# Kernel optimization log

Hardware: AMD Instinct MI355X
Metric: run time of the kernel (lower is better)

The kernel has to match this reference:

```python
import jax, jax.numpy as jnp
import numpy as np

N_NODES = 100000
NODES_PER_GRAPH = 200
N_GRAPHS = N_NODES // NODES_PER_GRAPH  # 500
N_EDGES = 3200000
NUM_FEATURES = 128
HIDDEN = 32
K_POOL = 50
NUM_CLASSES = 10
NUM_ITERATIONS = 3


def setup_inputs() -> dict:
    key = jax.random.key(0)
    ks = jax.random.split(key, 12)
    x = jax.random.normal(ks[0], (N_NODES, NUM_FEATURES), dtype=jnp.float32)
    edge_index = jax.random.randint(ks[1], (2, N_EDGES), 0, N_NODES, dtype=jnp.int64)
    batch = (jnp.arange(N_NODES, dtype=jnp.int64) // NODES_PER_GRAPH)
    # GCN weights (glorot-ish scale) + biases
    W1 = jax.random.normal(ks[2], (NUM_FEATURES, HIDDEN), dtype=jnp.float32) * (1.0 / np.sqrt(NUM_FEATURES))
    b1 = jnp.zeros((HIDDEN,), dtype=jnp.float32)
    W2 = jax.random.normal(ks[3], (HIDDEN, HIDDEN), dtype=jnp.float32) * (1.0 / np.sqrt(HIDDEN))
    b2 = jnp.zeros((HIDDEN,), dtype=jnp.float32)
    W3 = jax.random.normal(ks[4], (HIDDEN, HIDDEN), dtype=jnp.float32) * (1.0 / np.sqrt(HIDDEN))
    b3 = jnp.zeros((HIDDEN,), dtype=jnp.float32)
    # Capsule weights: [out_capsules, in_capsules, out_length, in_length]
    Wc1 = jax.random.normal(ks[5], (16, K_POOL, 32, 3 * HIDDEN), dtype=jnp.float32) * 0.05
    Wc2 = jax.random.normal(ks[6], (NUM_CLASSES, 16, 16, 32), dtype=jnp.float32) * 0.05
    return {"x": x, "edge_index": edge_index, "batch": batch,
            "W1": W1, "b1": b1, "W2": W2, "b2": b2, "W3": W3, "b3": b3,
            "Wc1": Wc1, "Wc2": Wc2}


def _gcn_conv(x, W, b, src, dst, mask):
    # PyG GCNConv: remove self-loops already done (mask), add self-loops, sym-normalize.
    h = x @ W  # [N, H]
    deg = jnp.zeros((x.shape[0],), dtype=h.dtype).at[dst].add(mask) + 1.0  # self-loop adds 1
    dinv = jax.lax.rsqrt(deg)
    norm = dinv[src] * dinv[dst] * mask  # [E]
    agg = jnp.zeros_like(h).at[dst].add(norm[:, None] * h[src])
    agg = agg + h * (dinv * dinv)[:, None]  # self-loop contribution h_i / deg_i
    return agg + b


def _squash(s, axis=-1):
    sq = jnp.sum(s * s, axis=axis, keepdims=True)
    return (sq / (1.0 + sq)) * s * jax.lax.rsqrt(sq + 1e-12)


def _capsule_linear(u, W, num_iterations):
    # u: [B, I, in_len]; W: [O, I, out_len, in_len]
    priors = jnp.einsum('oiLl,bil->boiL', W, u)  # [B, O, I, out_len]
    logits = jnp.zeros(priors.shape[:3] + (1,), dtype=priors.dtype)
    for it in range(num_iterations):
        c = jax.nn.softmax(logits, axis=1)             # over out capsules
        s = jnp.sum(c * priors, axis=2)                # [B, O, out_len]
        v = _squash(s)
        if it < num_iterations - 1:
            logits = logits + jnp.sum(priors * v[:, :, None, :], axis=-1, keepdims=True)
    return v


def _global_sort_pool(x, k):
    # x: [N, C], equal-size graphs -> [B, nper, C]; sort desc by last channel, take top-k
    xg = x.reshape(N_GRAPHS, NODES_PER_GRAPH, x.shape[-1])
    order = jnp.argsort(-xg[:, :, -1], axis=1)[:, :k]  # [B, k]
    return jnp.take_along_axis(xg, order[:, :, None], axis=1)  # [B, k, C]


def reference(x, edge_index, batch, W1, b1, W2, b2, W3, b3, Wc1, Wc2):
    src, dst = edge_index[0], edge_index[1]
    mask = (src != dst).astype(x.dtype)  # remove_self_loops
    x1 = jnp.tanh(_gcn_conv(x, W1, b1, src, dst, mask))
    x2 = jnp.tanh(_gcn_conv(x1, W2, b2, src, dst, mask))
    x3 = jnp.tanh(_gcn_conv(x2, W3, b3, src, dst, mask))
    xc = jnp.concatenate([x1, x2, x3], axis=-1)        # [N, 96]
    pooled = _global_sort_pool(xc, K_POOL)             # [B, 50, 96]
    out = _capsule_linear(pooled, Wc1, NUM_ITERATIONS)  # [B, 16, 32]
    out = _capsule_linear(out, Wc2, NUM_ITERATIONS)     # [B, 10, 16]
    return jnp.linalg.norm(out, axis=-1)                # [B, 10]
```

## Files before the change

### kernel.cpp

```cpp
#include <hip/hip_runtime.h>

#define NNODES 100000
#define NEDGES 3200000
#define NPG 200
#define NGRAPH 500
#define FIN 128
#define HID 32
#define KP 50
#define NCLS 10

#define NB1 196
#define BSH 9
#define CHUNK 8192
#define NBLK1 391

__global__ __launch_bounds__(512) void k_hist1(const int* __restrict__ src,
                                               const int* __restrict__ dst,
                                               int* __restrict__ totals) {
    __shared__ int hist[NB1];
    int t = threadIdx.x;
    for (int i = t; i < NB1; i += 512) hist[i] = 0;
    __syncthreads();
    int eb = blockIdx.x * CHUNK;
    for (int i = 0; i < CHUNK / 512; ++i) {
        int e = eb + t + i * 512;
        if (e < NEDGES) {
            int s = src[e], d = dst[e];
            if (s != d) atomicAdd(&hist[d >> BSH], 1);
        }
    }
    __syncthreads();
    for (int i = t; i < NB1; i += 512)
        if (hist[i]) atomicAdd(&totals[i], hist[i]);
}

__global__ __launch_bounds__(256) void k_scanb(const int* __restrict__ totals,
                                               int* __restrict__ bstart,
                                               int* __restrict__ cursor,
                                               int* __restrict__ offs) {
    __shared__ int lds[256];
    int t = threadIdx.x;
    int v = (t < NB1) ? totals[t] : 0;
    lds[t] = v;
    __syncthreads();
    for (int ofs = 1; ofs < 256; ofs <<= 1) {
        int add = (t >= ofs) ? lds[t - ofs] : 0;
        __syncthreads();
        lds[t] += add;
        __syncthreads();
    }
    if (t <= NB1) {
        int e = (t == 0) ? 0 : lds[t - 1];
        bstart[t] = e;
        if (t < NB1) cursor[t] = e;
    }
    if (t == 0) offs[NNODES] = lds[NB1 - 1];
}

__global__ __launch_bounds__(512) void k_place1(const int* __restrict__ src,
                                                const int* __restrict__ dst,
                                                int* __restrict__ cursor,
                                                unsigned* __restrict__ csorted) {
    __shared__ int hist[NB1];
    __shared__ int lstart[NB1];
    __shared__ int base[NB1];
    __shared__ int cnt2[NB1];
    __shared__ int sarr[256];
    __shared__ unsigned buf[CHUNK];
    __shared__ int dbuf[CHUNK];
    int t = threadIdx.x;
    for (int i = t; i < NB1; i += 512) { hist[i] = 0; cnt2[i] = 0; }
    __syncthreads();
    int eb = blockIdx.x * CHUNK;
    for (int i = 0; i < CHUNK / 512; ++i) {
        int e = eb + t + i * 512;
        if (e < NEDGES) {
            int s = src[e], d = dst[e];
            if (s != d) atomicAdd(&hist[d >> BSH], 1);
        }
    }
    __syncthreads();
    if (t < 256) sarr[t] = (t < NB1) ? hist[t] : 0;
    __syncthreads();
    for (int ofs = 1; ofs < 256; ofs <<= 1) {
        int add = (t < 256 && t >= ofs) ? sarr[t - ofs] : 0;
        __syncthreads();
        if (t < 256) sarr[t] += add;
        __syncthreads();
    }
    if (t < NB1) {
        lstart[t] = (t == 0) ? 0 : sarr[t - 1];
        base[t] = hist[t] ? atomicAdd(&cursor[t], hist[t]) : 0;
    }
    __syncthreads();
    for (int i = 0; i < CHUNK / 512; ++i) {
        int e = eb + t + i * 512;
        if (e < NEDGES) {
            int s = src[e], d = dst[e];
            if (s != d) {
                int bk = d >> BSH;
                int pos = atomicAdd(&cnt2[bk], 1);
                int slot = lstart[bk] + pos;
                buf[slot] = ((unsigned)s << BSH) | (unsigned)(d & 511);
                dbuf[slot] = base[bk] + pos;
            }
        }
    }
    __syncthreads();
    int nval = sarr[NB1 - 1];
    for (int j = t; j < nval; j += 512) csorted[dbuf[j]] = buf[j];
}

__global__ __launch_bounds__(512) void k_fill2(const int* __restrict__ bstart,
                                               const unsigned* __restrict__ csorted,
                                               int* __restrict__ csrc,
                                               int* __restrict__ offs,
                                               float* __restrict__ dinv) {
    __shared__ int cnt[512];
    __shared__ int loffs[512];
    __shared__ int cnt2[512];
    __shared__ int sarr[512];
    int b = blockIdx.x, t = threadIdx.x;
    cnt[t] = 0; cnt2[t] = 0;
    __syncthreads();
    int s0 = bstart[b], s1 = bstart[b + 1];
    for (int j = s0 + t; j < s1; j += 512) atomicAdd(&cnt[csorted[j] & 511], 1);
    __syncthreads();
    sarr[t] = cnt[t];
    __syncthreads();
    for (int ofs = 1; ofs < 512; ofs <<= 1) {
        int add = (t >= ofs) ? sarr[t - ofs] : 0;
        __syncthreads();
        sarr[t] += add;
        __syncthreads();
    }
    loffs[t] = sarr[t] - cnt[t];
    __syncthreads();
    int n = b * 512 + t;
    if (n < NNODES) {
        offs[n] = s0 + loffs[t];
        dinv[n] = rsqrtf((float)cnt[t] + 1.0f);
    }
    for (int j = s0 + t; j < s1; j += 512) {
        unsigned p = csorted[j];
        int d = p & 511;
        int pos = atomicAdd(&cnt2[d], 1);
        csrc[s0 + loffs[d] + pos] = (int)(p >> BSH);
    }
}

__global__ __launch_bounds__(256) void k_matmul(const float* __restrict__ X, int ldx, int K,
                                                const float* __restrict__ W,
                                                const float* __restrict__ dinv,
                                                float* __restrict__ h) {
    __shared__ float Wl[FIN * HID];
    __shared__ float Xl[64 * FIN];
    int t = threadIdx.x;
    for (int idx = t; idx < K * HID; idx += 256) Wl[idx] = W[idx];
    int n0 = blockIdx.x * 64;
    int ng = 64 * K / 4;
    for (int idx = t; idx < ng; idx += 256) {
        int r = (idx * 4) / K, c = (idx * 4) % K;
        float4 v = make_float4(0.f, 0.f, 0.f, 0.f);
        if (n0 + r < NNODES)
            v = *reinterpret_cast<const float4*>(X + (size_t)(n0 + r) * ldx + c);
        *reinterpret_cast<float4*>(&Xl[r * K + c]) = v;
    }
    __syncthreads();
    int j = t & 31, g = t >> 5;
    const float* xr = &Xl[(g * 8) * K];
    float a0 = 0, a1 = 0, a2 = 0, a3 = 0, a4 = 0, a5 = 0, a6 = 0, a7 = 0;
    for (int k = 0; k < K; ++k) {
        float w = Wl[k * HID + j];
        a0 += w * xr[0 * K + k];
        a1 += w * xr[1 * K + k];
        a2 += w * xr[2 * K + k];
        a3 += w * xr[3 * K + k];
        a4 += w * xr[4 * K + k];
        a5 += w * xr[5 * K + k];
        a6 += w * xr[6 * K + k];
        a7 += w * xr[7 * K + k];
    }
    int r0 = n0 + g * 8;
    float av[8] = {a0, a1, a2, a3, a4, a5, a6, a7};
    for (int q = 0; q < 8; ++q)
        if (r0 + q < NNODES) h[(size_t)(r0 + q) * HID + j] = av[q] * dinv[r0 + q];
}

__global__ __launch_bounds__(256) void k_gather(const int* __restrict__ offs,
                                                const int* __restrict__ csrc,
                                                const float* __restrict__ dinv,
                                                const float* __restrict__ hw,
                                                const float* __restrict__ bias,
                                                float* __restrict__ xc, int coloff) {
    int t = threadIdx.x;
    int n = blockIdx.x * 4 + (t >> 6);
    int lane = t & 63;
    int g = lane >> 3;
    int q = lane & 7;
    int beg = offs[n], end = offs[n + 1];
    int last = end - 1;
    float4 acc = make_float4(0.f, 0.f, 0.f, 0.f);
    for (int e0 = beg + g; e0 < end; e0 += 32) {
        int eB = e0 + 8, eC = e0 + 16, eD = e0 + 24;
        float mB = (eB <= last) ? 1.f : 0.f;
        float mC = (eC <= last) ? 1.f : 0.f;
        float mD = (eD <= last) ? 1.f : 0.f;
        int sA = csrc[e0];
        int sB = csrc[min(eB, last)];
        int sC = csrc[min(eC, last)];
        int sD = csrc[min(eD, last)];
        float4 hA = *reinterpret_cast<const float4*>(hw + (size_t)sA * HID + q * 4);
        float4 hB = *reinterpret_cast<const float4*>(hw + (size_t)sB * HID + q * 4);
        float4 hC = *reinterpret_cast<const float4*>(hw + (size_t)sC * HID + q * 4);
        float4 hD = *reinterpret_cast<const float4*>(hw + (size_t)sD * HID + q * 4);
        acc.x += hA.x; acc.y += hA.y; acc.z += hA.z; acc.w += hA.w;
        acc.x += mB * hB.x; acc.y += mB * hB.y; acc.z += mB * hB.z; acc.w += mB * hB.w;
        acc.x += mC * hC.x; acc.y += mC * hC.y; acc.z += mC * hC.z; acc.w += mC * hC.w;
        acc.x += mD * hD.x; acc.y += mD * hD.y; acc.z += mD * hD.z; acc.w += mD * hD.w;
    }
    for (int m = 8; m <= 32; m <<= 1) {
        acc.x += __shfl_xor(acc.x, m, 64);
        acc.y += __shfl_xor(acc.y, m, 64);
        acc.z += __shfl_xor(acc.z, m, 64);
        acc.w += __shfl_xor(acc.w, m, 64);
    }
    if (g == 0) {
        float di = dinv[n];
        float4 hv = *reinterpret_cast<const float4*>(hw + (size_t)n * HID + q * 4);
        float4 bv = *reinterpret_cast<const float4*>(bias + q * 4);
        float4 v;
        v.x = tanhf(di * (acc.x + hv.x) + bv.x);
        v.y = tanhf(di * (acc.y + hv.y) + bv.y);
        v.z = tanhf(di * (acc.z + hv.z) + bv.z);
        v.w = tanhf(di * (acc.w + hv.w) + bv.w);
        *reinterpret_cast<float4*>(xc + (size_t)n * 96 + coloff + q * 4) = v;
    }
}

__global__ __launch_bounds__(256) void k_sortpool(const float* __restrict__ xc,
                                                  float* __restrict__ pooled) {
    int g = blockIdx.x;
    __shared__ float vals[NPG];
    __shared__ int sel[KP];
    int t = threadIdx.x;
    if (t < NPG) vals[t] = xc[((size_t)g * NPG + t) * 96 + 95];
    __syncthreads();
    if (t < NPG) {
        float v = vals[t];
        int r = 0;
        for (int k = 0; k < NPG; ++k) {
            float vk = vals[k];
            r += (vk > v) || (vk == v && k < t);
        }
        if (r < KP) sel[r] = t;
    }
    __syncthreads();
    for (int idx = t; idx < KP * 24; idx += 256) {
        int r = idx / 24, c4 = (idx % 24) * 4;
        *reinterpret_cast<float4*>(pooled + (size_t)g * KP * 96 + r * 96 + c4) =
            *reinterpret_cast<const float4*>(xc + ((size_t)g * NPG + sel[r]) * 96 + c4);
    }
}

__global__ __launch_bounds__(512) void k_priors1(const float* __restrict__ pooled,
                                                 const float* __restrict__ Wc1,
                                                 float* __restrict__ priors) {
    int bid = blockIdx.x;
    int ct = bid & 3;
    int bt = (bid >> 2) & 1;
    int i = bid >> 3;
    __shared__ float As[48 * 256];
    __shared__ float Bs[48 * 128];
    int t = threadIdx.x;
    int tx = t & 15, ty = t >> 4;
    float acc[8][8];
#pragma unroll
    for (int r = 0; r < 8; ++r)
#pragma unroll
        for (int c = 0; c < 8; ++c) acc[r][c] = 0.f;

    for (int kh = 0; kh < 2; ++kh) {
        int kbase = kh * 48;
        __syncthreads();
        for (int idx = t; idx < 256 * 12; idx += 512) {
            int r = idx / 12, c4 = (idx % 12) * 4;
            int b = bt * 256 + r;
            float4 v = make_float4(0.f, 0.f, 0.f, 0.f);
            if (b < NGRAPH)
                v = *reinterpret_cast<const float4*>(pooled + ((size_t)b * KP + i) * 96 + kbase + c4);
            float vv[4] = {v.x, v.y, v.z, v.w};
#pragma unroll
            for (int j = 0; j < 4; ++j) {
                int k = c4 + j;
                int gp = (r >> 2) ^ ((k >> 2) & 31);
                As[k * 256 + gp * 4 + (r & 3)] = vv[j];
            }
        }
        for (int idx = t; idx < 128 * 12; idx += 512) {
            int c = idx / 12, c4 = (idx % 12) * 4;
            int col = ct * 128 + c;
            const float* wr = Wc1 + (((size_t)(col >> 5) * KP + i) * 32 + (col & 31)) * 96;
            float4 v = *reinterpret_cast<const float4*>(wr + kbase + c4);
            float vv[4] = {v.x, v.y, v.z, v.w};
#pragma unroll
            for (int j = 0; j < 4; ++j) {
                int k = c4 + j;
                int gp = (c >> 2) ^ ((k >> 2) & 31);
                Bs[k * 128 + gp * 4 + (c & 3)] = vv[j];
            }
        }
        __syncthreads();
        for (int k = 0; k < 48; ++k) {
            int key = (k >> 2) & 31;
            float4 a0 = *reinterpret_cast<const float4*>(&As[k * 256 + 4 * (ty ^ key)]);
            float4 a1 = *reinterpret_cast<const float4*>(&As[k * 256 + 4 * ((32 + ty) ^ key)]);
            float4 b0 = *reinterpret_cast<const float4*>(&Bs[k * 128 + 4 * (tx ^ key)]);
            float4 b1 = *reinterpret_cast<const float4*>(&Bs[k * 128 + 4 * ((16 + tx) ^ key)]);
            float a[8] = {a0.x, a0.y, a0.z, a0.w, a1.x, a1.y, a1.z, a1.w};
            float bb[8] = {b0.x, b0.y, b0.z, b0.w, b1.x, b1.y, b1.z, b1.w};
#pragma unroll
            for (int r = 0; r < 8; ++r)
#pragma unroll
                for (int c = 0; c < 8; ++c) acc[r][c] += a[r] * bb[c];
        }
    }
#pragma unroll
    for (int rh = 0; rh < 2; ++rh)
#pragma unroll
        for (int rr = 0; rr < 4; ++rr) {
            int b = bt * 256 + rh * 128 + ty * 4 + rr;
            if (b >= NGRAPH) continue;
#pragma unroll
            for (int ch = 0; ch < 2; ++ch) {
                int col = ct * 128 + ch * 64 + tx * 4;
                int o = col >> 5, L = col & 31;
                float4 v = make_float4(acc[rh * 4 + rr][ch * 4 + 0],
                                       acc[rh * 4 + rr][ch * 4 + 1],
                                       acc[rh * 4 + rr][ch * 4 + 2],
                                       acc[rh * 4 + rr][ch * 4 + 3]);
                *reinterpret_cast<float4*>(priors + (((size_t)b * 16 + o) * KP + i) * 32 + L) = v;
            }
        }
}

__global__ __launch_bounds__(256) void k_routing1(const float* __restrict__ priors_g,
                                                  float* __restrict__ v_out) {
    int b = blockIdx.x;
    __shared__ float P[16 * KP * 33];
    __shared__ float logits[16 * KP];
    __shared__ float c[16 * KP];
    __shared__ float s[16 * 32];
    __shared__ float v[16 * 32];
    __shared__ float scale[16];
    int t = threadIdx.x;
    const float* pg = priors_g + (size_t)b * (16 * KP * 32);
    for (int idx = t; idx < 16 * KP * 32; idx += 256)
        P[(idx >> 5) * 33 + (idx & 31)] = pg[idx];
    for (int idx = t; idx < 16 * KP; idx += 256) logits[idx] = 0.f;
    __syncthreads();
    for (int it = 0; it < 3; ++it) {
        if (t < KP) {
            float m = -1e30f;
            for (int o = 0; o < 16; ++o) m = fmaxf(m, logits[o * KP + t]);
            float sum = 0.f;
            for (int o = 0; o < 16; ++o) {
                float e = expf(logits[o * KP + t] - m);
                c[o * KP + t] = e;
                sum += e;
            }
            for (int o = 0; o < 16; ++o) c[o * KP + t] /= sum;
        }
        __syncthreads();
        for (int idx = t; idx < 16 * 32; idx += 256) {
            int o = idx >> 5, L = idx & 31;
            float acc = 0.f;
            for (int i = 0; i < KP; ++i) acc += c[o * KP + i] * P[(o * KP + i) * 33 + L];
            s[idx] = acc;
        }
        __syncthreads();
        if (t < 16) {
            float sq = 0.f;
            for (int L = 0; L < 32; ++L) sq += s[t * 32 + L] * s[t * 32 + L];
            scale[t] = (sq / (1.f + sq)) * (1.0f / sqrtf(sq + 1e-12f));
        }
        __syncthreads();
        for (int idx = t; idx < 16 * 32; idx += 256) v[idx] = s[idx] * scale[idx >> 5];
        __syncthreads();
        if (it < 2) {
            for (int idx = t; idx < 16 * KP; idx += 256) {
                int o = idx / KP, i = idx % KP;
                float acc = 0.f;
                for (int L = 0; L < 32; ++L) acc += P[(o * KP + i) * 33 + L] * v[o * 32 + L];
                logits[idx] += acc;
            }
            __syncthreads();
        }
    }
    for (int idx = t; idx < 16 * 32; idx += 256) v_out[(size_t)b * 512 + idx] = v[idx];
}

__global__ __launch_bounds__(256) void k_priors2(const float* __restrict__ v1,
                                                 const float* __restrict__ Wc2,
                                                 float* __restrict__ priors2) {
    int b = blockIdx.x;
    __shared__ float ul[16 * 32];
    int t = threadIdx.x;
    for (int idx = t; idx < 512; idx += 256) ul[idx] = v1[(size_t)b * 512 + idx];
    __syncthreads();
    for (int idx = t; idx < NCLS * 16 * 16; idx += 256) {
        int L = idx & 15, i = (idx >> 4) & 15, o = idx >> 8;
        const float* wr = Wc2 + ((size_t)((o * 16 + i) * 16 + L)) * 32;
        const float* ur = &ul[i * 32];
        float acc = 0.f;
        for (int l = 0; l < 32; ++l) acc += wr[l] * ur[l];
        priors2[(size_t)b * (NCLS * 16 * 16) + idx] = acc;
    }
}

__global__ __launch_bounds__(256) void k_routing2(const float* __restrict__ priors_g,
                                                  float* __restrict__ out) {
    int b = blockIdx.x;
    __shared__ float P[NCLS * 16 * 17];
    __shared__ float logits[NCLS * 16];
    __shared__ float c[NCLS * 16];
    __shared__ float s[NCLS * 16];
    __shared__ float v[NCLS * 16];
    __shared__ float scale[NCLS];
    int t = threadIdx.x;
    const float* pg = priors_g + (size_t)b * (NCLS * 16 * 16);
    for (int idx = t; idx < NCLS * 16 * 16; idx += 256)
        P[(idx >> 4) * 17 + (idx & 15)] = pg[idx];
    for (int idx = t; idx < NCLS * 16; idx += 256) logits[idx] = 0.f;
    __syncthreads();
    for (int it = 0; it < 3; ++it) {
        if (t < 16) {
            float m = -1e30f;
            for (int o = 0; o < NCLS; ++o) m = fmaxf(m, logits[o * 16 + t]);
            float sum = 0.f;
            for (int o = 0; o < NCLS; ++o) {
                float e = expf(logits[o * 16 + t] - m);
                c[o * 16 + t] = e;
                sum += e;
            }
            for (int o = 0; o < NCLS; ++o) c[o * 16 + t] /= sum;
        }
        __syncthreads();
        if (t < NCLS * 16) {
            int o = t >> 4, L = t & 15;
            float acc = 0.f;
            for (int i = 0; i < 16; ++i) acc += c[o * 16 + i] * P[(o * 16 + i) * 17 + L];
            s[t] = acc;
        }
        __syncthreads();
        if (t < NCLS) {
            float sq = 0.f;
            for (int L = 0; L < 16; ++L) sq += s[t * 16 + L] * s[t * 16 + L];
            scale[t] = (sq / (1.f + sq)) * (1.0f / sqrtf(sq + 1e-12f));
        }
        __syncthreads();
        if (t < NCLS * 16) v[t] = s[t] * scale[t >> 4];
        __syncthreads();
        if (it < 2) {
            if (t < NCLS * 16) {
                int o = t >> 4, i = t & 15;
                float acc = 0.f;
                for (int L = 0; L < 16; ++L) acc += P[(o * 16 + i) * 17 + L] * v[o * 16 + L];
                logits[t] += acc;
            }
            __syncthreads();
        }
    }
    if (t < NCLS) {
        float sq = 0.f;
        for (int L = 0; L < 16; ++L) sq += v[t * 16 + L] * v[t * 16 + L];
        out[(size_t)b * NCLS + t] = sqrtf(sq);
    }
}

extern "C" void kernel_launch(void* const* d_in, const int* in_sizes, int n_in,
                              void* d_out, int out_size, void* d_ws, size_t ws_size,
                              hipStream_t stream) {
    const float* x   = (const float*)d_in[0];
    const int*   ei  = (const int*)d_in[1];
    const float* W1  = (const float*)d_in[3];
    const float* b1  = (const float*)d_in[4];
    const float* W2  = (const float*)d_in[5];
    const float* b2  = (const float*)d_in[6];
    const float* W3  = (const float*)d_in[7];
    const float* b3  = (const float*)d_in[8];
    const float* Wc1 = (const float*)d_in[9];
    const float* Wc2 = (const float*)d_in[10];
    float* out = (float*)d_out;
    float* wsf = (float*)d_ws;

    const int* src = ei;
    const int* dst = ei + NEDGES;

    float*    xc      = wsf;
    float*    R       = wsf + 9600000;
    int*      totals  = (int*)R;
    int*      bstart  = (int*)(R + 200);
    int*      cursor  = (int*)(R + 400);
    float*    dinv    = R + 600;
    int*      offs    = (int*)(R + 100600);
    unsigned* csorted = (unsigned*)(R + 200608);
    int*      csrc    = (int*)(R + 3400608);
    float*    h       = R + 6600608;
    float*    pooled  = R + 200608;
    float*    pr1     = R + 9800608;
    float*    v1      = R + 22600608;
    float*    pr2     = R + 22856608;

    hipMemsetAsync(totals, 0, NB1 * sizeof(int), stream);
    k_hist1<<<NBLK1, 512, 0, stream>>>(src, dst, totals);
    k_scanb<<<1, 256, 0, stream>>>(totals, bstart, cursor, offs);
    k_place1<<<NBLK1, 512, 0, stream>>>(src, dst, cursor, csorted);
    k_fill2<<<NB1, 512, 0, stream>>>(bstart, csorted, csrc, offs, dinv);

    k_matmul<<<(NNODES + 63) / 64, 256, 0, stream>>>(x, FIN, FIN, W1, dinv, h);
    k_gather<<<NNODES / 4, 256, 0, stream>>>(offs, csrc, dinv, h, b1, xc, 0);
    k_matmul<<<(NNODES + 63) / 64, 256, 0, stream>>>(xc, 96, HID, W2, dinv, h);
    k_gather<<<NNODES / 4, 256, 0, stream>>>(offs, csrc, dinv, h, b2, xc, 32);
    k_matmul<<<(NNODES + 63) / 64, 256, 0, stream>>>(xc + 32, 96, HID, W3, dinv, h);
    k_gather<<<NNODES / 4, 256, 0, stream>>>(offs, csrc, dinv, h, b3, xc, 64);

    k_sortpool<<<NGRAPH, 256, 0, stream>>>(xc, pooled);
    k_priors1<<<KP * 8, 512, 0, stream>>>(pooled, Wc1, pr1);
    k_routing1<<<NGRAPH, 256, 0, stream>>>(pr1, v1);
    k_priors2<<<NGRAPH, 256, 0, stream>>>(v1, Wc2, pr2);
    k_routing2<<<NGRAPH, 256, 0, stream>>>(pr2, out);
}
```

Baseline: 416.7 us.

## Drop histogram pass via fixed-capacity buckets and pack two nodes per gather wave

Removes the global histogram and scan kernels by giving each destination bucket a fixed capacity region (CAP slots), so placement uses atomic cursors directly and the CSR stores begin/end pairs per node. The gather kernel now processes two nodes per 64-lane wave, with 4 edge groups per node and an 8-way unrolled loop. This saves a full pass over the edge list and two launches, at the cost of assuming no bucket exceeds CAP edges and leaving gaps in the edge arrays.

```diff
diff --git a/kernel.cpp b/kernel.cpp
--- a/kernel.cpp
+++ b/kernel.cpp
@@ -13,49 +13,7 @@
 #define BSH 9
 #define CHUNK 8192
 #define NBLK1 391
-
-__global__ __launch_bounds__(512) void k_hist1(const int* __restrict__ src,
-                                               const int* __restrict__ dst,
-                                               int* __restrict__ totals) {
-    __shared__ int hist[NB1];
-    int t = threadIdx.x;
-    for (int i = t; i < NB1; i += 512) hist[i] = 0;
-    __syncthreads();
-    int eb = blockIdx.x * CHUNK;
-    for (int i = 0; i < CHUNK / 512; ++i) {
-        int e = eb + t + i * 512;
-        if (e < NEDGES) {
-            int s = src[e], d = dst[e];
-            if (s != d) atomicAdd(&hist[d >> BSH], 1);
-        }
-    }
-    __syncthreads();
-    for (int i = t; i < NB1; i += 512)
-        if (hist[i]) atomicAdd(&totals[i], hist[i]);
-}
-
-__global__ __launch_bounds__(256) void k_scanb(const int* __restrict__ totals,
-                                               int* __restrict__ bstart,
-                                               int* __restrict__ cursor,
-                                               int* __restrict__ offs) {
-    __shared__ int lds[256];
-    int t = threadIdx.x;
-    int v = (t < NB1) ? totals[t] : 0;
-    lds[t] = v;
-    __syncthreads();
-    for (int ofs = 1; ofs < 256; ofs <<= 1) {
-        int add = (t >= ofs) ? lds[t - ofs] : 0;
-        __syncthreads();
-        lds[t] += add;
-        __syncthreads();
-    }
-    if (t <= NB1) {
-        int e = (t == 0) ? 0 : lds[t - 1];
-        bstart[t] = e;
-        if (t < NB1) cursor[t] = e;
-    }
-    if (t == 0) offs[NNODES] = lds[NB1 - 1];
-}
+#define CAP 17408
 
 __global__ __launch_bounds__(512) void k_place1(const int* __restrict__ src,
                                                 const int* __restrict__ dst,
@@ -90,7 +48,7 @@
     }
     if (t < NB1) {
         lstart[t] = (t == 0) ? 0 : sarr[t - 1];
-        base[t] = hist[t] ? atomicAdd(&cursor[t], hist[t]) : 0;
+        base[t] = hist[t] ? (t * CAP + atomicAdd(&cursor[t], hist[t])) : 0;
     }
     __syncthreads();
     for (int i = 0; i < CHUNK / 512; ++i) {
@@ -111,10 +69,10 @@
     for (int j = t; j < nval; j += 512) csorted[dbuf[j]] = buf[j];
 }
 
-__global__ __launch_bounds__(512) void k_fill2(const int* __restrict__ bstart,
+__global__ __launch_bounds__(512) void k_fill2(const int* __restrict__ cursor,
                                                const unsigned* __restrict__ csorted,
                                                int* __restrict__ csrc,
-                                               int* __restrict__ offs,
+                                               int2* __restrict__ begend,
                                                float* __restrict__ dinv) {
     __shared__ int cnt[512];
     __shared__ int loffs[512];
@@ -123,8 +81,9 @@
     int b = blockIdx.x, t = threadIdx.x;
     cnt[t] = 0; cnt2[t] = 0;
     __syncthreads();
-    int s0 = bstart[b], s1 = bstart[b + 1];
-    for (int j = s0 + t; j < s1; j += 512) atomicAdd(&cnt[csorted[j] & 511], 1);
+    int base = b * CAP;
+    int m = cursor[b];
+    for (int j = t; j < m; j += 512) atomicAdd(&cnt[csorted[base + j] & 511], 1);
     __syncthreads();
     sarr[t] = cnt[t];
     __syncthreads();
@@ -138,14 +97,15 @@
     __syncthreads();
     int n = b * 512 + t;
     if (n < NNODES) {
-        offs[n] = s0 + loffs[t];
+        int beg = base + loffs[t];
+        begend[n] = make_int2(beg, beg + cnt[t]);
         dinv[n] = rsqrtf((float)cnt[t] + 1.0f);
     }
-    for (int j = s0 + t; j < s1; j += 512) {
-        unsigned p = csorted[j];
+    for (int j = t; j < m; j += 512) {
+        unsigned p = csorted[base + j];
         int d = p & 511;
         int pos = atomicAdd(&cnt2[d], 1);
-        csrc[s0 + loffs[d] + pos] = (int)(p >> BSH);
+        csrc[base + loffs[d] + pos] = (int)(p >> BSH);
     }
 }
 
@@ -187,39 +147,34 @@
         if (r0 + q < NNODES) h[(size_t)(r0 + q) * HID + j] = av[q] * dinv[r0 + q];
 }
 
-__global__ __launch_bounds__(256) void k_gather(const int* __restrict__ offs,
+__global__ __launch_bounds__(256) void k_gather(const int2* __restrict__ begend,
                                                 const int* __restrict__ csrc,
                                                 const float* __restrict__ dinv,
                                                 const float* __restrict__ hw,
                                                 const float* __restrict__ bias,
                                                 float* __restrict__ xc, int coloff) {
     int t = threadIdx.x;
-    int n = blockIdx.x * 4 + (t >> 6);
+    int wv = t >> 6;
     int lane = t & 63;
-    int g = lane >> 3;
-    int q = lane & 7;
-    int beg = offs[n], end = offs[n + 1];
-    int last = end - 1;
+    int nh = lane >> 5;
+    int sub = lane & 31;
+    int g = sub >> 3;
+    int q = sub & 7;
+    int n = blockIdx.x * 8 + wv * 2 + nh;
+    int2 be = begend[n];
+    int beg = be.x, end = be.y, last = end - 1;
     float4 acc = make_float4(0.f, 0.f, 0.f, 0.f);
     for (int e0 = beg + g; e0 < end; e0 += 32) {
-        int eB = e0 + 8, eC = e0 + 16, eD = e0 + 24;
-        float mB = (eB <= last) ? 1.f : 0.f;
-        float mC = (eC <= last) ? 1.f : 0.f;
-        float mD = (eD <= last) ? 1.f : 0.f;
-        int sA = csrc[e0];
-        int sB = csrc[min(eB, last)];
-        int sC = csrc[min(eC, last)];
-        int sD = csrc[min(eD, last)];
-        float4 hA = *reinterpret_cast<const float4*>(hw + (size_t)sA * HID + q * 4);
-        float4 hB = *reinterpret_cast<const float4*>(hw + (size_t)sB * HID + q * 4);
-        float4 hC = *reinterpret_cast<const float4*>(hw + (size_t)sC * HID + q * 4);
-        float4 hD = *reinterpret_cast<const float4*>(hw + (size_t)sD * HID + q * 4);
-        acc.x += hA.x; acc.y += hA.y; acc.z += hA.z; acc.w += hA.w;
-        acc.x += mB * hB.x; acc.y += mB * hB.y; acc.z += mB * hB.z; acc.w += mB * hB.w;
-        acc.x += mC * hC.x; acc.y += mC * hC.y; acc.z += mC * hC.z; acc.w += mC * hC.w;
-        acc.x += mD * hD.x; acc.y += mD * hD.y; acc.z += mD * hD.z; acc.w += mD * hD.w;
-    }
-    for (int m = 8; m <= 32; m <<= 1) {
+#pragma unroll
+        for (int j = 0; j < 8; ++j) {
+            int e = e0 + 4 * j;
+            float mk = (e <= last) ? 1.f : 0.f;
+            int s = csrc[min(e, last)];
+            float4 hv = *reinterpret_cast<const float4*>(hw + (size_t)s * HID + q * 4);
+            acc.x += mk * hv.x; acc.y += mk * hv.y; acc.z += mk * hv.z; acc.w += mk * hv.w;
+        }
+    }
+    for (int m = 8; m <= 16; m <<= 1) {
         acc.x += __shfl_xor(acc.x, m, 64);
         acc.y += __shfl_xor(acc.y, m, 64);
         acc.z += __shfl_xor(acc.z, m, 64);
@@ -497,33 +452,30 @@
     const int* src = ei;
     const int* dst = ei + NEDGES;
 
-    float*    xc      = wsf;
-    float*    R       = wsf + 9600000;
-    int*      totals  = (int*)R;
-    int*      bstart  = (int*)(R + 200);
-    int*      cursor  = (int*)(R + 400);
-    float*    dinv    = R + 600;
-    int*      offs    = (int*)(R + 100600);
-    unsigned* csorted = (unsigned*)(R + 200608);
-    int*      csrc    = (int*)(R + 3400608);
-    float*    h       = R + 6600608;
-    float*    pooled  = R + 200608;
-    float*    pr1     = R + 9800608;
-    float*    v1      = R + 22600608;
-    float*    pr2     = R + 22856608;
-
-    hipMemsetAsync(totals, 0, NB1 * sizeof(int), stream);
-    k_hist1<<<NBLK1, 512, 0, stream>>>(src, dst, totals);
-    k_scanb<<<1, 256, 0, stream>>>(totals, bstart, cursor, offs);
+    float* xc = wsf;
+    float* R  = wsf + 9600000;
+    int*   cursor  = (int*)R;
+    float* dinv    = R + 256;
+    int2*  begend  = (int2*)(R + 100256);
+    float* A       = R + 300256;
+    unsigned* csorted = (unsigned*)A;
+    float* h       = A;
+    float* pooled  = A;
+    int*   csrc    = (int*)(R + 3712224);
+    float* pr1     = R + 7124192;
+    float* v1      = R + 19924192;
+    float* pr2     = R + 20180192;
+
+    hipMemsetAsync(cursor, 0, 256 * sizeof(int), stream);
     k_place1<<<NBLK1, 512, 0, stream>>>(src, dst, cursor, csorted);
-    k_fill2<<<NB1, 512, 0, stream>>>(bstart, csorted, csrc, offs, dinv);
+    k_fill2<<<NB1, 512, 0, stream>>>(cursor, csorted, csrc, begend, dinv);
 
     k_matmul<<<(NNODES + 63) / 64, 256, 0, stream>>>(x, FIN, FIN, W1, dinv, h);
-    k_gather<<<NNODES / 4, 256, 0, stream>>>(offs, csrc, dinv, h, b1, xc, 0);
+    k_gather<<<NNODES / 8, 256, 0, stream>>>(begend, csrc, dinv, h, b1, xc, 0);
     k_matmul<<<(NNODES + 63) / 64, 256, 0, stream>>>(xc, 96, HID, W2, dinv, h);
-    k_gather<<<NNODES / 4, 256, 0, stream>>>(offs, csrc, dinv, h, b2, xc, 32);
+    k_gather<<<NNODES / 8, 256, 0, stream>>>(begend, csrc, dinv, h, b2, xc, 32);
     k_matmul<<<(NNODES + 63) / 64, 256, 0, stream>>>(xc + 32, 96, HID, W3, dinv, h);
-    k_gather<<<NNODES / 4, 256, 0, stream>>>(offs, csrc, dinv, h, b3, xc, 64);
+    k_gather<<<NNODES / 8, 256, 0, stream>>>(begend, csrc, dinv, h, b3, xc, 64);
 
     k_sortpool<<<NGRAPH, 256, 0, stream>>>(xc, pooled);
     k_priors1<<<KP * 8, 512, 0, stream>>>(pooled, Wc1, pr1);
```

New measurement: 394.5 us. 5.3% less time.
